# Kernel optimization log

Measured on AMD Instinct MI355X. Metric: run time of the kernel, lower is better.

## Reference

```python
import jax, jax.numpy as jnp
import numpy as np

DIM = 320
HEADS = 8
D_HEAD = 40
CTX_DIM = 768
INNER_FF = 4 * DIM  # 1280
EPS = 1e-5


def _ln(x, w, b):
    mu = jnp.mean(x, axis=-1, keepdims=True)
    var = jnp.mean(jnp.square(x - mu), axis=-1, keepdims=True)
    return (x - mu) * jax.lax.rsqrt(var + EPS) * w + b


def _attn(xq, ctx, Wq, Wk, Wv, Wo, bo):
    # Wq: [dim, inner]; Wk/Wv: [ctx_dim, inner]; Wo: [inner, dim]
    b, n, _ = xq.shape
    m = ctx.shape[1]
    scale = D_HEAD ** -0.5
    q = (xq @ Wq).reshape(b, n, HEADS, D_HEAD)
    k = (ctx @ Wk).reshape(b, m, HEADS, D_HEAD)
    v = (ctx @ Wv).reshape(b, m, HEADS, D_HEAD)
    sim = jnp.einsum('bihd,bjhd->bhij', q, k) * scale
    attn = jax.nn.softmax(sim, axis=-1)
    out = jnp.einsum('bhij,bjhd->bihd', attn, v).reshape(b, n, HEADS * D_HEAD)
    return out @ Wo + bo


def setup_inputs() -> dict:
    key = jax.random.key(0)
    ks = jax.random.split(key, 20)
    s = 0.02
    inner = HEADS * D_HEAD  # 320
    d = {
        'x': jax.random.normal(ks[0], (2, 4096, DIM), jnp.float32),
        'context': jax.random.normal(ks[1], (2, 77, CTX_DIM), jnp.float32),
        # norm params
        'ln1_w': jnp.ones((DIM,)), 'ln1_b': jnp.zeros((DIM,)),
        'ln2_w': jnp.ones((DIM,)), 'ln2_b': jnp.zeros((DIM,)),
        'ln3_w': jnp.ones((DIM,)), 'ln3_b': jnp.zeros((DIM,)),
        # attn1 (self)
        'a1_Wq': jax.random.normal(ks[2], (DIM, inner)) * s,
        'a1_Wk': jax.random.normal(ks[3], (DIM, inner)) * s,
        'a1_Wv': jax.random.normal(ks[4], (DIM, inner)) * s,
        'a1_Wo': jax.random.normal(ks[5], (inner, DIM)) * s,
        'a1_bo': jnp.zeros((DIM,)),
        # attn2 (cross)
        'a2_Wq': jax.random.normal(ks[6], (DIM, inner)) * s,
        'a2_Wk': jax.random.normal(ks[7], (CTX_DIM, inner)) * s,
        'a2_Wv': jax.random.normal(ks[8], (CTX_DIM, inner)) * s,
        'a2_Wo': jax.random.normal(ks[9], (inner, DIM)) * s,
        'a2_bo': jnp.zeros((DIM,)),
        # GEGLU feed-forward
        'ff_W1': jax.random.normal(ks[10], (DIM, 2 * INNER_FF)) * s,
        'ff_b1': jnp.zeros((2 * INNER_FF,)),
        'ff_W2': jax.random.normal(ks[11], (INNER_FF, DIM)) * s,
        'ff_b2': jnp.zeros((DIM,)),
    }
    return d


def reference(x, context, ln1_w, ln1_b, ln2_w, ln2_b, ln3_w, ln3_b,
              a1_Wq, a1_Wk, a1_Wv, a1_Wo, a1_bo,
              a2_Wq, a2_Wk, a2_Wv, a2_Wo, a2_bo,
              ff_W1, ff_b1, ff_W2, ff_b2):
    h = _ln(x, ln1_w, ln1_b)
    x = _attn(h, h, a1_Wq, a1_Wk, a1_Wv, a1_Wo, a1_bo) + x
    h = _ln(x, ln2_w, ln2_b)
    x = _attn(h, context, a2_Wq, a2_Wk, a2_Wv, a2_Wo, a2_bo) + x
    h = _ln(x, ln3_w, ln3_b)
    proj = h @ ff_W1 + ff_b1
    u, gate = jnp.split(proj, 2, axis=-1)
    ff = (u * jax.nn.gelu(gate, approximate=False)) @ ff_W2 + ff_b2
    return ff + x
```

## Files before the change

kernel.cpp:

```cpp
#include <hip/hip_runtime.h>
#include <hip/hip_bf16.h>
#include <math.h>

typedef __hip_bfloat16 bf16;
typedef __attribute__((ext_vector_type(8))) short bf16x8;
typedef __attribute__((ext_vector_type(4))) short bf16x4;
typedef __attribute__((ext_vector_type(4))) float f32x4;
typedef __attribute__((ext_vector_type(2))) unsigned int u32x2;

#define DIM 320
#define HEADS 8
#define DHEAD 40
#define CTXD 768
#define FFI 1280
#define NQ 4096
#define NCTX 77
#define BATCH 2

static __device__ __forceinline__ short f2bs(float v) {
    union { bf16 b; short s; } x; x.b = __float2bfloat16(v); return x.s;
}
static __device__ __forceinline__ unsigned pkbf(float hi, float lo) {
    return __builtin_amdgcn_perm(__float_as_uint(hi), __float_as_uint(lo), 0x07060302u);
}

__global__ void __launch_bounds__(256) wtrans_all(
    const float* q1s, const float* k1s, const float* v1s, const float* o1s,
    const float* q2s, const float* o2s, const float* k2s, const float* v2s,
    const float* w1s, const float* w2s,
    short* q1d, short* k1d, short* v1d, short* o1d,
    short* q2d, short* o2d, short* k2d, short* v2d,
    short* w1d, short* w2d)
{
    int bid = blockIdx.x;
    const float* W; short* Wt; int K, N, base;
    if (bid < 600) {
        int ws = bid / 100; base = bid % 100; K = DIM; N = DIM;
        W  = ws == 0 ? q1s : ws == 1 ? k1s : ws == 2 ? v1s : ws == 3 ? o1s : ws == 4 ? q2s : o2s;
        Wt = ws == 0 ? q1d : ws == 1 ? k1d : ws == 2 ? v1d : ws == 3 ? o1d : ws == 4 ? q2d : o2d;
    } else if (bid < 1080) {
        int i = bid - 600; int ws = i / 240; base = i % 240; K = CTXD; N = DIM;
        W = ws ? v2s : k2s; Wt = ws ? v2d : k2d;
    } else if (bid < 1880) {
        base = bid - 1080; K = DIM; N = 2 * FFI; W = w1s; Wt = w1d;
    } else {
        base = bid - 1880; K = FFI; N = DIM; W = w2s; Wt = w2d;
    }
    int ntx = N / 32;
    int n0 = (base % ntx) * 32, k0 = (base / ntx) * 32;
    __shared__ float T[32][33];
    int c = threadIdx.x & 31, r8 = threadIdx.x >> 5;
#pragma unroll
    for (int rr = 0; rr < 4; ++rr) {
        int r = r8 + rr * 8;
        T[r][c] = W[(size_t)(k0 + r) * N + n0 + c];
    }
    __syncthreads();
#pragma unroll
    for (int rr = 0; rr < 4; ++rr) {
        int r = r8 + rr * 8;
        Wt[(size_t)(n0 + r) * K + k0 + c] = f2bs(T[c][r]);
    }
}

__global__ void __launch_bounds__(256) ln_kernel(const float* __restrict__ src,
                          const float* __restrict__ w, const float* __restrict__ bp,
                          short* __restrict__ out, int rows)
{
    int row = blockIdx.x * 4 + (threadIdx.x >> 6);
    int lane = threadIdx.x & 63;
    if (row >= rows) return;
    float v[5];
    float s = 0.f, s2 = 0.f;
#pragma unroll
    for (int t = 0; t < 5; ++t) {
        int c = lane + t * 64;
        float x = src[(size_t)row * DIM + c];
        v[t] = x; s += x; s2 += x * x;
    }
#pragma unroll
    for (int off = 32; off; off >>= 1) { s += __shfl_xor(s, off); s2 += __shfl_xor(s2, off); }
    float mean = s * (1.f / DIM);
    float var = s2 * (1.f / DIM) - mean * mean;
    float rstd = rsqrtf(var + 1e-5f);
#pragma unroll
    for (int t = 0; t < 5; ++t) {
        int c = lane + t * 64;
        out[(size_t)row * DIM + c] = f2bs((v[t] - mean) * rstd * w[c] + bp[c]);
    }
}

__global__ void __launch_bounds__(256) mfma_qkv(const short* __restrict__ A,
                          const short* __restrict__ wq, const short* __restrict__ wk,
                          const short* __restrict__ wv,
                          short* __restrict__ qb, short* __restrict__ kbuf,
                          short* __restrict__ vts, float qscale)
{
    __shared__ short As[64 * 72];
    __shared__ short Bs[64 * 72];
    const int tid = threadIdx.x;
    const int z = blockIdx.z;
    const short* Wt = z == 0 ? wq : z == 1 ? wk : wv;
    const int w = tid >> 6, lane = tid & 63, lrow = lane & 15, lgrp = lane >> 4;
    const int m0 = blockIdx.y * 64, n0 = blockIdx.x * 64;
    f32x4 acc[4] = {};
    for (int kb = 0; kb < DIM / 64; ++kb) {
        const int k0 = kb << 6;
        __syncthreads();
#pragma unroll
        for (int l = 0; l < 2; ++l) {
            int idx = tid + (l << 8);
            int arow = idx >> 3, ac = idx & 7;
            *(bf16x8*)&As[arow * 72 + ac * 8] =
                *(const bf16x8*)(A + (size_t)(m0 + arow) * DIM + k0 + ac * 8);
            *(bf16x8*)&Bs[arow * 72 + ac * 8] =
                *(const bf16x8*)(Wt + (size_t)(n0 + arow) * DIM + k0 + ac * 8);
        }
        __syncthreads();
#pragma unroll
        for (int s = 0; s < 2; ++s) {
            bf16x8 a = *(const bf16x8*)&As[(w * 16 + lrow) * 72 + s * 32 + lgrp * 8];
#pragma unroll
            for (int ct = 0; ct < 4; ++ct) {
                bf16x8 b = *(const bf16x8*)&Bs[(ct * 16 + lrow) * 72 + s * 32 + lgrp * 8];
                acc[ct] = __builtin_amdgcn_mfma_f32_16x16x32_bf16(a, b, acc[ct], 0, 0, 0);
            }
        }
    }
#pragma unroll
    for (int ct = 0; ct < 4; ++ct) {
        int col = n0 + ct * 16 + lrow;
        if (z == 2) {
            int row0 = m0 + w * 16 + lgrp * 4;
            int b_ = row0 >> 12, kv = row0 & (NQ - 1);
            int hh = col / DHEAD, d = col - hh * DHEAD;
            bf16x4 pv;
#pragma unroll
            for (int r = 0; r < 4; ++r) pv[r] = f2bs(acc[ct][r]);
            *(bf16x4*)(vts + (size_t)((b_ * HEADS + hh) * 48 + d) * NQ + kv) = pv;
        } else {
#pragma unroll
            for (int r = 0; r < 4; ++r) {
                int row = m0 + w * 16 + lgrp * 4 + r;
                float v = acc[ct][r];
                if (z == 0) qb[(size_t)row * DIM + col] = f2bs(v * qscale);
                else        kbuf[(size_t)row * DIM + col] = f2bs(v);
            }
        }
    }
}

__global__ void __launch_bounds__(256) mfma_crosskv(const float* __restrict__ ctx,
                          const short* __restrict__ wk2, const short* __restrict__ wv2,
                          short* __restrict__ k2, short* __restrict__ vt2)
{
    __shared__ short As[64 * 72];
    __shared__ short Bs[64 * 72];
    const int tid = threadIdx.x;
    const int z = blockIdx.z;
    const short* Wt = z ? wv2 : wk2;
    const int Mc = BATCH * NCTX;
    const int w = tid >> 6, lane = tid & 63, lrow = lane & 15, lgrp = lane >> 4;
    const int m0 = blockIdx.y * 64, n0 = blockIdx.x * 64;
    f32x4 acc[4] = {};
    for (int kb = 0; kb < CTXD / 64; ++kb) {
        const int k0 = kb << 6;
        __syncthreads();
#pragma unroll
        for (int l = 0; l < 2; ++l) {
            int idx = tid + (l << 8);
            int arow = idx >> 3, ac = idx & 7;
            int grow = m0 + arow;
            bf16x8 v = {};
            if (grow < Mc) {
                const float* Af = ctx + (size_t)grow * CTXD + k0 + ac * 8;
#pragma unroll
                for (int j = 0; j < 8; ++j) v[j] = f2bs(Af[j]);
            }
            *(bf16x8*)&As[arow * 72 + ac * 8] = v;
            *(bf16x8*)&Bs[arow * 72 + ac * 8] =
                *(const bf16x8*)(Wt + (size_t)(n0 + arow) * CTXD + k0 + ac * 8);
        }
        __syncthreads();
#pragma unroll
        for (int s = 0; s < 2; ++s) {
            bf16x8 a = *(const bf16x8*)&As[(w * 16 + lrow) * 72 + s * 32 + lgrp * 8];
#pragma unroll
            for (int ct = 0; ct < 4; ++ct) {
                bf16x8 b = *(const bf16x8*)&Bs[(ct * 16 + lrow) * 72 + s * 32 + lgrp * 8];
                acc[ct] = __builtin_amdgcn_mfma_f32_16x16x32_bf16(a, b, acc[ct], 0, 0, 0);
            }
        }
    }
#pragma unroll
    for (int ct = 0; ct < 4; ++ct) {
        int col = n0 + ct * 16 + lrow;
#pragma unroll
        for (int r = 0; r < 4; ++r) {
            int row = m0 + w * 16 + lgrp * 4 + r;
            if (row >= Mc) continue;
            float v = acc[ct][r];
            if (z == 0) k2[(size_t)row * DIM + col] = f2bs(v);
            else {
                int b_ = row / NCTX, kv = row - b_ * NCTX;
                int hh = col / DHEAD, d = col - hh * DHEAD;
                vt2[(size_t)((b_ * HEADS + hh) * 48 + d) * 128 + kv] = f2bs(v);
            }
        }
    }
}

template<int MODE>
__global__ void __launch_bounds__(256) mfma_gemm(const short* __restrict__ A,
                          const short* __restrict__ Wt,
                          const float* __restrict__ bias,
                          const float* __restrict__ res,
                          float* __restrict__ xbuf,
                          short* __restrict__ outb,
                          float* __restrict__ outf,
                          int M, int N, int K, float oscale)
{
    __shared__ short As[64 * 72];
    __shared__ short Bs[64 * 72];
    const int tid = threadIdx.x;
    const int w = tid >> 6, lane = tid & 63, lrow = lane & 15, lgrp = lane >> 4;
    const int m0 = blockIdx.y * 64, n0 = blockIdx.x * 64;
    f32x4 acc[4] = {};
    const int kiters = K >> 6;
    for (int kb = 0; kb < kiters; ++kb) {
        const int k0 = kb << 6;
        __syncthreads();
#pragma unroll
        for (int l = 0; l < 2; ++l) {
            int idx = tid + (l << 8);
            int arow = idx >> 3, ac = idx & 7;
            *(bf16x8*)&As[arow * 72 + ac * 8] =
                *(const bf16x8*)(A + (size_t)(m0 + arow) * K + k0 + ac * 8);
            *(bf16x8*)&Bs[arow * 72 + ac * 8] =
                *(const bf16x8*)(Wt + (size_t)(n0 + arow) * K + k0 + ac * 8);
        }
        __syncthreads();
#pragma unroll
        for (int s = 0; s < 2; ++s) {
            bf16x8 a = *(const bf16x8*)&As[(w * 16 + lrow) * 72 + s * 32 + lgrp * 8];
#pragma unroll
            for (int ct = 0; ct < 4; ++ct) {
                bf16x8 b = *(const bf16x8*)&Bs[(ct * 16 + lrow) * 72 + s * 32 + lgrp * 8];
                acc[ct] = __builtin_amdgcn_mfma_f32_16x16x32_bf16(a, b, acc[ct], 0, 0, 0);
            }
        }
    }
#pragma unroll
    for (int ct = 0; ct < 4; ++ct) {
        int col = n0 + ct * 16 + lrow;
        float bvx = bias ? bias[col] : 0.f;
#pragma unroll
        for (int r = 0; r < 4; ++r) {
            int row = m0 + w * 16 + lgrp * 4 + r;
            float v = acc[ct][r] + bvx;
            size_t o = (size_t)row * N + col;
            if (MODE == 0)      outb[o] = f2bs(v * oscale);
            else if (MODE == 1) xbuf[o] = v + res[o];
            else if (MODE == 2) xbuf[o] += v;
            else                outf[o] = v + xbuf[o];
        }
    }
}

__global__ void __launch_bounds__(256) mfma_geglu(const short* __restrict__ A,
                           const short* __restrict__ Wt1,
                           const float* __restrict__ b1, short* __restrict__ G)
{
    __shared__ short As[64 * 72];
    __shared__ short Bu[64 * 72];
    __shared__ short Bg[64 * 72];
    const int tid = threadIdx.x;
    const int w = tid >> 6, lane = tid & 63, lrow = lane & 15, lgrp = lane >> 4;
    const int m0 = blockIdx.y * 64, n0 = blockIdx.x * 64;
    f32x4 au[4] = {}, ag[4] = {};
    for (int kb = 0; kb < DIM / 64; ++kb) {
        const int k0 = kb << 6;
        __syncthreads();
#pragma unroll
        for (int l = 0; l < 2; ++l) {
            int idx = tid + (l << 8);
            int arow = idx >> 3, ac = idx & 7;
            *(bf16x8*)&As[arow * 72 + ac * 8] =
                *(const bf16x8*)(A + (size_t)(m0 + arow) * DIM + k0 + ac * 8);
            *(bf16x8*)&Bu[arow * 72 + ac * 8] =
                *(const bf16x8*)(Wt1 + (size_t)(n0 + arow) * DIM + k0 + ac * 8);
            *(bf16x8*)&Bg[arow * 72 + ac * 8] =
                *(const bf16x8*)(Wt1 + (size_t)(FFI + n0 + arow) * DIM + k0 + ac * 8);
        }
        __syncthreads();
#pragma unroll
        for (int s = 0; s < 2; ++s) {
            bf16x8 a = *(const bf16x8*)&As[(w * 16 + lrow) * 72 + s * 32 + lgrp * 8];
#pragma unroll
            for (int ct = 0; ct < 4; ++ct) {
                bf16x8 bu = *(const bf16x8*)&Bu[(ct * 16 + lrow) * 72 + s * 32 + lgrp * 8];
                au[ct] = __builtin_amdgcn_mfma_f32_16x16x32_bf16(a, bu, au[ct], 0, 0, 0);
                bf16x8 bg = *(const bf16x8*)&Bg[(ct * 16 + lrow) * 72 + s * 32 + lgrp * 8];
                ag[ct] = __builtin_amdgcn_mfma_f32_16x16x32_bf16(a, bg, ag[ct], 0, 0, 0);
            }
        }
    }
#pragma unroll
    for (int ct = 0; ct < 4; ++ct) {
        int col = n0 + ct * 16 + lrow;
        float bu = b1[col], bg = b1[FFI + col];
#pragma unroll
        for (int r = 0; r < 4; ++r) {
            int row = m0 + w * 16 + lgrp * 4 + r;
            float u = au[ct][r] + bu;
            float g = ag[ct][r] + bg;
            float gelu = 0.5f * g * (1.f + erff(g * 0.70710678f));
            G[(size_t)row * FFI + col] = f2bs(u * gelu);
        }
    }
}

template<bool FULL>
__global__ void __launch_bounds__(512) flash_mfma(const short* __restrict__ Q,
                           const short* __restrict__ Kb,
                           const short* __restrict__ VtG,
                           short* __restrict__ O,
                           int kvlen, int kvs)
{
    __shared__ short Ks[2][64 * 64];
    __shared__ short Vt[2][48 * 64];
    __shared__ short Ps[128 * 64];
    const int tid = threadIdx.x;
    const int w = tid >> 6, lane = tid & 63, lrow = lane & 15, lgrp = lane >> 4;
    const int hh = blockIdx.y, b = blockIdx.z;
    const int q0 = blockIdx.x * 128;
    const int swz = (lrow & 7) << 4;

    if (tid < 512) { ((bf16x8*)Ks[0])[tid] = (bf16x8){}; ((bf16x8*)Ks[1])[tid] = (bf16x8){}; }
    if (tid < 384) {
        short fill = ((tid >> 3) == 40) ? (short)0x3F80 : (short)0;
        bf16x8 f8 = {fill, fill, fill, fill, fill, fill, fill, fill};
        ((bf16x8*)Vt[0])[tid] = f8; ((bf16x8*)Vt[1])[tid] = f8;
    }

    const size_t qbase = ((size_t)(b * NQ + q0 + w * 16 + lrow)) * DIM + hh * DHEAD;
    bf16x8 bq0 = *(const bf16x8*)(Q + qbase + lgrp * 8);
    bf16x8 bq1 = {};
    if (lgrp == 0) bq1 = *(const bf16x8*)(Q + qbase + 32);

    const bool isK = tid < 320;
    const int kv0 = isK ? tid / 5 : 0, cc0 = isK ? tid % 5 : 0;
    const int vc0 = tid - 320;
    const int vd0 = vc0 >> 3, vcc0 = vc0 & 7;
    const bool hasV1 = tid < 192;
    const int vd1 = (192 + tid) >> 3, vcc1 = (192 + tid) & 7;
    const bool wrV1 = hasV1 && (vd1 < DHEAD);

    bf16x8 st0, st1;
    const size_t kbase = (size_t)b * kvlen;
    const size_t vbase = (size_t)((b * HEADS + hh) * 48);

    auto issue = [&](int t) {
        const int j0 = t << 6;
        st0 = (bf16x8){};
        if (isK) {
            if (FULL || j0 + kv0 < kvlen)
                st0 = *(const bf16x8*)(Kb + (kbase + j0 + kv0) * DIM + hh * DHEAD + cc0 * 8);
        } else {
            st0 = *(const bf16x8*)(VtG + (vbase + vd0) * kvs + j0 + vcc0 * 8);
            if (!FULL && j0 + 63 >= kvlen) {
#pragma unroll
                for (int j = 0; j < 8; ++j) if (j0 + vcc0 * 8 + j >= kvlen) st0[j] = 0;
            }
        }
        if (wrV1) {
            st1 = *(const bf16x8*)(VtG + (vbase + vd1) * kvs + j0 + vcc1 * 8);
            if (!FULL && j0 + 63 >= kvlen) {
#pragma unroll
                for (int j = 0; j < 8; ++j) if (j0 + vcc1 * 8 + j >= kvlen) st1[j] = 0;
            }
        }
    };
    auto commit = [&](int bi) {
        if (isK)
            *(bf16x8*)((char*)Ks[bi] + kv0 * 128 + ((cc0 * 16) ^ ((kv0 & 7) << 4))) = st0;
        else
            *(bf16x8*)((char*)Vt[bi] + vd0 * 128 + ((vcc0 * 16) ^ ((vd0 & 7) << 4))) = st0;
        if (wrV1)
            *(bf16x8*)((char*)Vt[bi] + vd1 * 128 + ((vcc1 * 16) ^ ((vd1 & 7) << 4))) = st1;
    };

    f32x4 o_acc[3] = {};

    issue(0);
    __syncthreads();
    commit(0);
    const int ntiles = (kvlen + 63) >> 6;
    char* prow = (char*)Ps + (w * 16 + lrow) * 128;
    for (int t = 0; t < ntiles; ++t) {
        const int j0 = t << 6;
        const int bi = t & 1;
        __syncthreads();
        if (t + 1 < ntiles) issue(t + 1);

        f32x4 sacc[4] = {};
#pragma unroll
        for (int ct = 0; ct < 4; ++ct) {
            const char* krow = (char*)Ks[bi] + (ct * 16 + lrow) * 128;
            bf16x8 ak0 = *(const bf16x8*)(krow + ((lgrp * 16) ^ swz));
            sacc[ct] = __builtin_amdgcn_mfma_f32_16x16x32_bf16(ak0, bq0, sacc[ct], 0, 0, 0);
            bf16x8 ak1 = *(const bf16x8*)(krow + ((64 + lgrp * 16) ^ swz));
            sacc[ct] = __builtin_amdgcn_mfma_f32_16x16x32_bf16(ak1, bq1, sacc[ct], 0, 0, 0);
        }
        if (!FULL && j0 + 64 > kvlen) {
#pragma unroll
            for (int ct = 0; ct < 4; ++ct)
#pragma unroll
                for (int r = 0; r < 4; ++r)
                    if (j0 + ct * 16 + lgrp * 4 + r >= kvlen) sacc[ct][r] = -1e30f;
        }
#pragma unroll
        for (int ct = 0; ct < 4; ++ct) {
            float p0 = __builtin_amdgcn_exp2f(sacc[ct][0]);
            float p1 = __builtin_amdgcn_exp2f(sacc[ct][1]);
            float p2 = __builtin_amdgcn_exp2f(sacc[ct][2]);
            float p3 = __builtin_amdgcn_exp2f(sacc[ct][3]);
            u32x2 pk; pk[0] = pkbf(p1, p0); pk[1] = pkbf(p3, p2);
            *(u32x2*)(prow + ((ct * 32 + lgrp * 8) ^ swz)) = pk;
        }
#pragma unroll
        for (int s = 0; s < 2; ++s) {
            bf16x8 bp = *(const bf16x8*)(prow + ((s * 64 + lgrp * 16) ^ swz));
#pragma unroll
            for (int dt = 0; dt < 3; ++dt) {
                bf16x8 av = *(const bf16x8*)((char*)Vt[bi] + (dt * 16 + lrow) * 128 + ((s * 64 + lgrp * 16) ^ swz));
                o_acc[dt] = __builtin_amdgcn_mfma_f32_16x16x32_bf16(av, bp, o_acc[dt], 0, 0, 0);
            }
        }
        if (t + 1 < ntiles) commit((t + 1) & 1);
    }
    float lsum = __shfl(o_acc[2][0], 32 + (lane & 15));
    float invl = 1.f / lsum;
    const size_t obase = ((size_t)(b * NQ + q0 + w * 16 + lrow)) * DIM + hh * DHEAD;
#pragma unroll
    for (int dt = 0; dt < 3; ++dt) {
        int dbase = dt * 16 + lgrp * 4;
        if (dbase < DHEAD) {
            u32x2 ov;
            ov[0] = pkbf(o_acc[dt][1] * invl, o_acc[dt][0] * invl);
            ov[1] = pkbf(o_acc[dt][3] * invl, o_acc[dt][2] * invl);
            *(u32x2*)(O + obase + dbase) = ov;
        }
    }
}

extern "C" void kernel_launch(void* const* d_in, const int* in_sizes, int n_in,
                              void* d_out, int out_size, void* d_ws, size_t ws_size,
                              hipStream_t stream)
{
    const float* x      = (const float*)d_in[0];
    const float* ctx    = (const float*)d_in[1];
    const float* ln1_w  = (const float*)d_in[2];
    const float* ln1_b  = (const float*)d_in[3];
    const float* ln2_w  = (const float*)d_in[4];
    const float* ln2_b  = (const float*)d_in[5];
    const float* ln3_w  = (const float*)d_in[6];
    const float* ln3_b  = (const float*)d_in[7];
    const float* a1_Wq  = (const float*)d_in[8];
    const float* a1_Wk  = (const float*)d_in[9];
    const float* a1_Wv  = (const float*)d_in[10];
    const float* a1_Wo  = (const float*)d_in[11];
    const float* a1_bo  = (const float*)d_in[12];
    const float* a2_Wq  = (const float*)d_in[13];
    const float* a2_Wk  = (const float*)d_in[14];
    const float* a2_Wv  = (const float*)d_in[15];
    const float* a2_Wo  = (const float*)d_in[16];
    const float* a2_bo  = (const float*)d_in[17];
    const float* ff_W1  = (const float*)d_in[18];
    const float* ff_b1  = (const float*)d_in[19];
    const float* ff_W2  = (const float*)d_in[20];
    const float* ff_b2  = (const float*)d_in[21];

    const int M = BATCH * NQ;
    const float qscale2 = (float)(0.15811388300841898 * 1.4426950408889634);

    char* p = (char*)d_ws;
    auto carve = [&](size_t bytes) { char* r = p; p += (bytes + 255) & ~255ULL; return r; };
    short* h       = (short*)carve((size_t)M * DIM * 2);
    short* qb      = (short*)carve((size_t)M * DIM * 2);
    short* kbuf    = (short*)carve((size_t)M * DIM * 2);
    short* attnout = (short*)carve((size_t)M * DIM * 2);
    float* xbuf    = (float*)carve((size_t)M * DIM * 4);
    short* gbuf    = (short*)carve((size_t)M * FFI * 2);
    short* VtS     = (short*)carve((size_t)BATCH * HEADS * 48 * NQ * 2);
    short* Vt2     = (short*)carve((size_t)BATCH * HEADS * 48 * 128 * 2);
    short* k2      = (short*)carve((size_t)256 * DIM * 2);
    short* wtq1    = (short*)carve((size_t)DIM * DIM * 2);
    short* wtk1    = (short*)carve((size_t)DIM * DIM * 2);
    short* wtv1    = (short*)carve((size_t)DIM * DIM * 2);
    short* wto1    = (short*)carve((size_t)DIM * DIM * 2);
    short* wtq2    = (short*)carve((size_t)DIM * DIM * 2);
    short* wto2    = (short*)carve((size_t)DIM * DIM * 2);
    short* wtk2    = (short*)carve((size_t)DIM * CTXD * 2);
    short* wtv2    = (short*)carve((size_t)DIM * CTXD * 2);
    short* wt1     = (short*)carve((size_t)2 * FFI * DIM * 2);
    short* wt2     = (short*)carve((size_t)DIM * FFI * 2);

    dim3 blk(256);
    dim3 g320(DIM / 64, M / 64);
    dim3 gattn(NQ / 128, HEADS, BATCH);

    wtrans_all<<<2280, blk, 0, stream>>>(a1_Wq, a1_Wk, a1_Wv, a1_Wo, a2_Wq, a2_Wo,
                                         a2_Wk, a2_Wv, ff_W1, ff_W2,
                                         wtq1, wtk1, wtv1, wto1, wtq2, wto2,
                                         wtk2, wtv2, wt1, wt2);
    ln_kernel<<<M / 4, blk, 0, stream>>>(x, ln1_w, ln1_b, h, M);
    mfma_qkv<<<dim3(5, 128, 3), blk, 0, stream>>>(h, wtq1, wtk1, wtv1, qb, kbuf, VtS, qscale2);
    flash_mfma<true><<<gattn, dim3(512), 0, stream>>>(qb, kbuf, VtS, attnout, NQ, NQ);
    mfma_gemm<1><<<g320, blk, 0, stream>>>(attnout, wto1, a1_bo, x, xbuf, nullptr, nullptr, M, DIM, DIM, 1.f);
    ln_kernel<<<M / 4, blk, 0, stream>>>(xbuf, ln2_w, ln2_b, h, M);
    mfma_gemm<0><<<g320, blk, 0, stream>>>(h, wtq2, nullptr, nullptr, nullptr, qb, nullptr, M, DIM, DIM, qscale2);
    mfma_crosskv<<<dim3(5, 3, 2), blk, 0, stream>>>(ctx, wtk2, wtv2, k2, Vt2);
    flash_mfma<false><<<gattn, dim3(512), 0, stream>>>(qb, k2, Vt2, attnout, NCTX, 128);
    mfma_gemm<2><<<g320, blk, 0, stream>>>(attnout, wto2, a2_bo, nullptr, xbuf, nullptr, nullptr, M, DIM, DIM, 1.f);
    ln_kernel<<<M / 4, blk, 0, stream>>>(xbuf, ln3_w, ln3_b, h, M);
    mfma_geglu<<<dim3(FFI / 64, M / 64), blk, 0, stream>>>(h, wt1, ff_b1, gbuf);
    mfma_gemm<3><<<g320, blk, 0, stream>>>(gbuf, wt2, ff_b2, nullptr, xbuf, nullptr, (float*)d_out, M, DIM, FFI, 1.f);
}
```

Before: 249.3 us.

## Enlarge GEMM tiles to 128x64 with 2x2 wave layout; add MFMA priority hints

All dense GEMM kernels (QKV, output projections, GEGLU, FF2) move from 64x64 tiles, where each wave computed a 16x64 strip, to 128x64 tiles. Waves are now arranged 2x2 and each computes a 64x32 sub-tile, so B fragments are reused across four A fragments and the M grid is halved. This is meant to cut global and LDS traffic per MFMA, at the cost of more accumulator registers and fewer blocks. The flash attention kernel also raises wave priority around its MFMA sections using s_setprio.

```diff
diff --git a/kernel.cpp b/kernel.cpp
--- a/kernel.cpp
+++ b/kernel.cpp
@@ -90,61 +90,203 @@
     }
 }
 
-__global__ void __launch_bounds__(256) mfma_qkv(const short* __restrict__ A,
+
+template<int MODE>
+__global__ void __launch_bounds__(256) gemm128(const short* __restrict__ A,
+                          const short* __restrict__ Wt,
+                          const float* __restrict__ bias,
+                          const float* __restrict__ res,
+                          float* __restrict__ xbuf,
+                          short* __restrict__ outb,
+                          float* __restrict__ outf,
+                          int N, int K, float oscale)
+{
+    __shared__ short As[128 * 72];
+    __shared__ short Bs[64 * 72];
+    const int tid = threadIdx.x;
+    const int w = tid >> 6, lane = tid & 63, lrow = lane & 15, lgrp = lane >> 4;
+    const int wr = w >> 1, wc = w & 1;
+    const int m0 = blockIdx.y * 128, n0 = blockIdx.x * 64;
+    f32x4 acc[4][2] = {};
+    for (int k0 = 0; k0 < K; k0 += 64) {
+        __syncthreads();
+#pragma unroll
+        for (int l = 0; l < 4; ++l) {
+            int idx = tid + (l << 8);
+            int arow = idx >> 3, ac = idx & 7;
+            *(bf16x8*)&As[arow * 72 + ac * 8] =
+                *(const bf16x8*)(A + (size_t)(m0 + arow) * K + k0 + ac * 8);
+        }
+#pragma unroll
+        for (int l = 0; l < 2; ++l) {
+            int idx = tid + (l << 8);
+            int brow = idx >> 3, bc = idx & 7;
+            *(bf16x8*)&Bs[brow * 72 + bc * 8] =
+                *(const bf16x8*)(Wt + (size_t)(n0 + brow) * K + k0 + bc * 8);
+        }
+        __syncthreads();
+#pragma unroll
+        for (int s = 0; s < 2; ++s) {
+            bf16x8 b0 = *(const bf16x8*)&Bs[(wc * 32 + lrow) * 72 + s * 32 + lgrp * 8];
+            bf16x8 b1 = *(const bf16x8*)&Bs[(wc * 32 + 16 + lrow) * 72 + s * 32 + lgrp * 8];
+#pragma unroll
+            for (int m = 0; m < 4; ++m) {
+                bf16x8 a = *(const bf16x8*)&As[(wr * 64 + m * 16 + lrow) * 72 + s * 32 + lgrp * 8];
+                acc[m][0] = __builtin_amdgcn_mfma_f32_16x16x32_bf16(a, b0, acc[m][0], 0, 0, 0);
+                acc[m][1] = __builtin_amdgcn_mfma_f32_16x16x32_bf16(a, b1, acc[m][1], 0, 0, 0);
+            }
+        }
+    }
+#pragma unroll
+    for (int n = 0; n < 2; ++n) {
+        int col = n0 + wc * 32 + n * 16 + lrow;
+        float bvx = bias ? bias[col] : 0.f;
+#pragma unroll
+        for (int m = 0; m < 4; ++m) {
+#pragma unroll
+            for (int r = 0; r < 4; ++r) {
+                int row = m0 + wr * 64 + m * 16 + lgrp * 4 + r;
+                float v = acc[m][n][r] + bvx;
+                size_t o = (size_t)row * N + col;
+                if (MODE == 0)      outb[o] = f2bs(v * oscale);
+                else if (MODE == 1) xbuf[o] = v + res[o];
+                else if (MODE == 2) xbuf[o] += v;
+                else                outf[o] = v + xbuf[o];
+            }
+        }
+    }
+}
+
+__global__ void __launch_bounds__(256) qkv128(const short* __restrict__ A,
                           const short* __restrict__ wq, const short* __restrict__ wk,
                           const short* __restrict__ wv,
                           short* __restrict__ qb, short* __restrict__ kbuf,
                           short* __restrict__ vts, float qscale)
 {
-    __shared__ short As[64 * 72];
+    __shared__ short As[128 * 72];
     __shared__ short Bs[64 * 72];
     const int tid = threadIdx.x;
     const int z = blockIdx.z;
     const short* Wt = z == 0 ? wq : z == 1 ? wk : wv;
     const int w = tid >> 6, lane = tid & 63, lrow = lane & 15, lgrp = lane >> 4;
-    const int m0 = blockIdx.y * 64, n0 = blockIdx.x * 64;
-    f32x4 acc[4] = {};
-    for (int kb = 0; kb < DIM / 64; ++kb) {
-        const int k0 = kb << 6;
-        __syncthreads();
-#pragma unroll
-        for (int l = 0; l < 2; ++l) {
+    const int wr = w >> 1, wc = w & 1;
+    const int m0 = blockIdx.y * 128, n0 = blockIdx.x * 64;
+    f32x4 acc[4][2] = {};
+    for (int k0 = 0; k0 < DIM; k0 += 64) {
+        __syncthreads();
+#pragma unroll
+        for (int l = 0; l < 4; ++l) {
             int idx = tid + (l << 8);
             int arow = idx >> 3, ac = idx & 7;
             *(bf16x8*)&As[arow * 72 + ac * 8] =
                 *(const bf16x8*)(A + (size_t)(m0 + arow) * DIM + k0 + ac * 8);
-            *(bf16x8*)&Bs[arow * 72 + ac * 8] =
-                *(const bf16x8*)(Wt + (size_t)(n0 + arow) * DIM + k0 + ac * 8);
+        }
+#pragma unroll
+        for (int l = 0; l < 2; ++l) {
+            int idx = tid + (l << 8);
+            int brow = idx >> 3, bc = idx & 7;
+            *(bf16x8*)&Bs[brow * 72 + bc * 8] =
+                *(const bf16x8*)(Wt + (size_t)(n0 + brow) * DIM + k0 + bc * 8);
         }
         __syncthreads();
 #pragma unroll
         for (int s = 0; s < 2; ++s) {
-            bf16x8 a = *(const bf16x8*)&As[(w * 16 + lrow) * 72 + s * 32 + lgrp * 8];
-#pragma unroll
-            for (int ct = 0; ct < 4; ++ct) {
-                bf16x8 b = *(const bf16x8*)&Bs[(ct * 16 + lrow) * 72 + s * 32 + lgrp * 8];
-                acc[ct] = __builtin_amdgcn_mfma_f32_16x16x32_bf16(a, b, acc[ct], 0, 0, 0);
-            }
-        }
-    }
-#pragma unroll
-    for (int ct = 0; ct < 4; ++ct) {
-        int col = n0 + ct * 16 + lrow;
-        if (z == 2) {
-            int row0 = m0 + w * 16 + lgrp * 4;
-            int b_ = row0 >> 12, kv = row0 & (NQ - 1);
-            int hh = col / DHEAD, d = col - hh * DHEAD;
-            bf16x4 pv;
-#pragma unroll
-            for (int r = 0; r < 4; ++r) pv[r] = f2bs(acc[ct][r]);
-            *(bf16x4*)(vts + (size_t)((b_ * HEADS + hh) * 48 + d) * NQ + kv) = pv;
-        } else {
+            bf16x8 b0 = *(const bf16x8*)&Bs[(wc * 32 + lrow) * 72 + s * 32 + lgrp * 8];
+            bf16x8 b1 = *(const bf16x8*)&Bs[(wc * 32 + 16 + lrow) * 72 + s * 32 + lgrp * 8];
+#pragma unroll
+            for (int m = 0; m < 4; ++m) {
+                bf16x8 a = *(const bf16x8*)&As[(wr * 64 + m * 16 + lrow) * 72 + s * 32 + lgrp * 8];
+                acc[m][0] = __builtin_amdgcn_mfma_f32_16x16x32_bf16(a, b0, acc[m][0], 0, 0, 0);
+                acc[m][1] = __builtin_amdgcn_mfma_f32_16x16x32_bf16(a, b1, acc[m][1], 0, 0, 0);
+            }
+        }
+    }
+#pragma unroll
+    for (int n = 0; n < 2; ++n) {
+        int col = n0 + wc * 32 + n * 16 + lrow;
+#pragma unroll
+        for (int m = 0; m < 4; ++m) {
+            if (z == 2) {
+                int row0 = m0 + wr * 64 + m * 16 + lgrp * 4;
+                int b_ = row0 >> 12, kv = row0 & (NQ - 1);
+                int hh = col / DHEAD, d = col - hh * DHEAD;
+                bf16x4 pv;
+#pragma unroll
+                for (int r = 0; r < 4; ++r) pv[r] = f2bs(acc[m][n][r]);
+                *(bf16x4*)(vts + (size_t)((b_ * HEADS + hh) * 48 + d) * NQ + kv) = pv;
+            } else {
+#pragma unroll
+                for (int r = 0; r < 4; ++r) {
+                    int row = m0 + wr * 64 + m * 16 + lgrp * 4 + r;
+                    float v = acc[m][n][r];
+                    if (z == 0) qb[(size_t)row * DIM + col] = f2bs(v * qscale);
+                    else        kbuf[(size_t)row * DIM + col] = f2bs(v);
+                }
+            }
+        }
+    }
+}
+
+__global__ void __launch_bounds__(256) geglu128(const short* __restrict__ A,
+                           const short* __restrict__ Wt1,
+                           const float* __restrict__ b1, short* __restrict__ G)
+{
+    __shared__ short As[128 * 72];
+    __shared__ short Bu[64 * 72];
+    __shared__ short Bg[64 * 72];
+    const int tid = threadIdx.x;
+    const int w = tid >> 6, lane = tid & 63, lrow = lane & 15, lgrp = lane >> 4;
+    const int wr = w >> 1, wc = w & 1;
+    const int m0 = blockIdx.y * 128, n0 = blockIdx.x * 64;
+    f32x4 au[4][2] = {}, ag[4][2] = {};
+    for (int k0 = 0; k0 < DIM; k0 += 64) {
+        __syncthreads();
+#pragma unroll
+        for (int l = 0; l < 4; ++l) {
+            int idx = tid + (l << 8);
+            int arow = idx >> 3, ac = idx & 7;
+            *(bf16x8*)&As[arow * 72 + ac * 8] =
+                *(const bf16x8*)(A + (size_t)(m0 + arow) * DIM + k0 + ac * 8);
+        }
+#pragma unroll
+        for (int l = 0; l < 2; ++l) {
+            int idx = tid + (l << 8);
+            int brow = idx >> 3, bc = idx & 7;
+            *(bf16x8*)&Bu[brow * 72 + bc * 8] =
+                *(const bf16x8*)(Wt1 + (size_t)(n0 + brow) * DIM + k0 + bc * 8);
+            *(bf16x8*)&Bg[brow * 72 + bc * 8] =
+                *(const bf16x8*)(Wt1 + (size_t)(FFI + n0 + brow) * DIM + k0 + bc * 8);
+        }
+        __syncthreads();
+#pragma unroll
+        for (int s = 0; s < 2; ++s) {
+            bf16x8 bu0 = *(const bf16x8*)&Bu[(wc * 32 + lrow) * 72 + s * 32 + lgrp * 8];
+            bf16x8 bu1 = *(const bf16x8*)&Bu[(wc * 32 + 16 + lrow) * 72 + s * 32 + lgrp * 8];
+            bf16x8 bg0 = *(const bf16x8*)&Bg[(wc * 32 + lrow) * 72 + s * 32 + lgrp * 8];
+            bf16x8 bg1 = *(const bf16x8*)&Bg[(wc * 32 + 16 + lrow) * 72 + s * 32 + lgrp * 8];
+#pragma unroll
+            for (int m = 0; m < 4; ++m) {
+                bf16x8 a = *(const bf16x8*)&As[(wr * 64 + m * 16 + lrow) * 72 + s * 32 + lgrp * 8];
+                au[m][0] = __builtin_amdgcn_mfma_f32_16x16x32_bf16(a, bu0, au[m][0], 0, 0, 0);
+                au[m][1] = __builtin_amdgcn_mfma_f32_16x16x32_bf16(a, bu1, au[m][1], 0, 0, 0);
+                ag[m][0] = __builtin_amdgcn_mfma_f32_16x16x32_bf16(a, bg0, ag[m][0], 0, 0, 0);
+                ag[m][1] = __builtin_amdgcn_mfma_f32_16x16x32_bf16(a, bg1, ag[m][1], 0, 0, 0);
+            }
+        }
+    }
+#pragma unroll
+    for (int n = 0; n < 2; ++n) {
+        int col = n0 + wc * 32 + n * 16 + lrow;
+        float bu = b1[col], bg = b1[FFI + col];
+#pragma unroll
+        for (int m = 0; m < 4; ++m) {
 #pragma unroll
             for (int r = 0; r < 4; ++r) {
-                int row = m0 + w * 16 + lgrp * 4 + r;
-                float v = acc[ct][r];
-                if (z == 0) qb[(size_t)row * DIM + col] = f2bs(v * qscale);
-                else        kbuf[(size_t)row * DIM + col] = f2bs(v);
+                int row = m0 + wr * 64 + m * 16 + lgrp * 4 + r;
+                float u = au[m][n][r] + bu;
+                float g = ag[m][n][r] + bg;
+                float gelu = 0.5f * g * (1.f + erff(g * 0.70710678f));
+                G[(size_t)row * FFI + col] = f2bs(u * gelu);
             }
         }
     }
@@ -210,116 +352,6 @@
     }
 }
 
-template<int MODE>
-__global__ void __launch_bounds__(256) mfma_gemm(const short* __restrict__ A,
-                          const short* __restrict__ Wt,
-                          const float* __restrict__ bias,
-                          const float* __restrict__ res,
-                          float* __restrict__ xbuf,
-                          short* __restrict__ outb,
-                          float* __restrict__ outf,
-                          int M, int N, int K, float oscale)
-{
-    __shared__ short As[64 * 72];
-    __shared__ short Bs[64 * 72];
-    const int tid = threadIdx.x;
-    const int w = tid >> 6, lane = tid & 63, lrow = lane & 15, lgrp = lane >> 4;
-    const int m0 = blockIdx.y * 64, n0 = blockIdx.x * 64;
-    f32x4 acc[4] = {};
-    const int kiters = K >> 6;
-    for (int kb = 0; kb < kiters; ++kb) {
-        const int k0 = kb << 6;
-        __syncthreads();
-#pragma unroll
-        for (int l = 0; l < 2; ++l) {
-            int idx = tid + (l << 8);
-            int arow = idx >> 3, ac = idx & 7;
-            *(bf16x8*)&As[arow * 72 + ac * 8] =
-                *(const bf16x8*)(A + (size_t)(m0 + arow) * K + k0 + ac * 8);
-            *(bf16x8*)&Bs[arow * 72 + ac * 8] =
-                *(const bf16x8*)(Wt + (size_t)(n0 + arow) * K + k0 + ac * 8);
-        }
-        __syncthreads();
-#pragma unroll
-        for (int s = 0; s < 2; ++s) {
-            bf16x8 a = *(const bf16x8*)&As[(w * 16 + lrow) * 72 + s * 32 + lgrp * 8];
-#pragma unroll
-            for (int ct = 0; ct < 4; ++ct) {
-                bf16x8 b = *(const bf16x8*)&Bs[(ct * 16 + lrow) * 72 + s * 32 + lgrp * 8];
-                acc[ct] = __builtin_amdgcn_mfma_f32_16x16x32_bf16(a, b, acc[ct], 0, 0, 0);
-            }
-        }
-    }
-#pragma unroll
-    for (int ct = 0; ct < 4; ++ct) {
-        int col = n0 + ct * 16 + lrow;
-        float bvx = bias ? bias[col] : 0.f;
-#pragma unroll
-        for (int r = 0; r < 4; ++r) {
-            int row = m0 + w * 16 + lgrp * 4 + r;
-            float v = acc[ct][r] + bvx;
-            size_t o = (size_t)row * N + col;
-            if (MODE == 0)      outb[o] = f2bs(v * oscale);
-            else if (MODE == 1) xbuf[o] = v + res[o];
-            else if (MODE == 2) xbuf[o] += v;
-            else                outf[o] = v + xbuf[o];
-        }
-    }
-}
-
-__global__ void __launch_bounds__(256) mfma_geglu(const short* __restrict__ A,
-                           const short* __restrict__ Wt1,
-                           const float* __restrict__ b1, short* __restrict__ G)
-{
-    __shared__ short As[64 * 72];
-    __shared__ short Bu[64 * 72];
-    __shared__ short Bg[64 * 72];
-    const int tid = threadIdx.x;
-    const int w = tid >> 6, lane = tid & 63, lrow = lane & 15, lgrp = lane >> 4;
-    const int m0 = blockIdx.y * 64, n0 = blockIdx.x * 64;
-    f32x4 au[4] = {}, ag[4] = {};
-    for (int kb = 0; kb < DIM / 64; ++kb) {
-        const int k0 = kb << 6;
-        __syncthreads();
-#pragma unroll
-        for (int l = 0; l < 2; ++l) {
-            int idx = tid + (l << 8);
-            int arow = idx >> 3, ac = idx & 7;
-            *(bf16x8*)&As[arow * 72 + ac * 8] =
-                *(const bf16x8*)(A + (size_t)(m0 + arow) * DIM + k0 + ac * 8);
-            *(bf16x8*)&Bu[arow * 72 + ac * 8] =
-                *(const bf16x8*)(Wt1 + (size_t)(n0 + arow) * DIM + k0 + ac * 8);
-            *(bf16x8*)&Bg[arow * 72 + ac * 8] =
-                *(const bf16x8*)(Wt1 + (size_t)(FFI + n0 + arow) * DIM + k0 + ac * 8);
-        }
-        __syncthreads();
-#pragma unroll
-        for (int s = 0; s < 2; ++s) {
-            bf16x8 a = *(const bf16x8*)&As[(w * 16 + lrow) * 72 + s * 32 + lgrp * 8];
-#pragma unroll
-            for (int ct = 0; ct < 4; ++ct) {
-                bf16x8 bu = *(const bf16x8*)&Bu[(ct * 16 + lrow) * 72 + s * 32 + lgrp * 8];
-                au[ct] = __builtin_amdgcn_mfma_f32_16x16x32_bf16(a, bu, au[ct], 0, 0, 0);
-                bf16x8 bg = *(const bf16x8*)&Bg[(ct * 16 + lrow) * 72 + s * 32 + lgrp * 8];
-                ag[ct] = __builtin_amdgcn_mfma_f32_16x16x32_bf16(a, bg, ag[ct], 0, 0, 0);
-            }
-        }
-    }
-#pragma unroll
-    for (int ct = 0; ct < 4; ++ct) {
-        int col = n0 + ct * 16 + lrow;
-        float bu = b1[col], bg = b1[FFI + col];
-#pragma unroll
-        for (int r = 0; r < 4; ++r) {
-            int row = m0 + w * 16 + lgrp * 4 + r;
-            float u = au[ct][r] + bu;
-            float g = ag[ct][r] + bg;
-            float gelu = 0.5f * g * (1.f + erff(g * 0.70710678f));
-            G[(size_t)row * FFI + col] = f2bs(u * gelu);
-        }
-    }
-}
-
 template<bool FULL>
 __global__ void __launch_bounds__(512) flash_mfma(const short* __restrict__ Q,
                            const short* __restrict__ Kb,
@@ -404,6 +436,7 @@
         if (t + 1 < ntiles) issue(t + 1);
 
         f32x4 sacc[4] = {};
+        __builtin_amdgcn_s_setprio(1);
 #pragma unroll
         for (int ct = 0; ct < 4; ++ct) {
             const char* krow = (char*)Ks[bi] + (ct * 16 + lrow) * 128;
@@ -412,6 +445,7 @@
             bf16x8 ak1 = *(const bf16x8*)(krow + ((64 + lgrp * 16) ^ swz));
             sacc[ct] = __builtin_amdgcn_mfma_f32_16x16x32_bf16(ak1, bq1, sacc[ct], 0, 0, 0);
         }
+        __builtin_amdgcn_s_setprio(0);
         if (!FULL && j0 + 64 > kvlen) {
 #pragma unroll
             for (int ct = 0; ct < 4; ++ct)
@@ -428,6 +462,7 @@
             u32x2 pk; pk[0] = pkbf(p1, p0); pk[1] = pkbf(p3, p2);
             *(u32x2*)(prow + ((ct * 32 + lgrp * 8) ^ swz)) = pk;
         }
+        __builtin_amdgcn_s_setprio(1);
 #pragma unroll
         for (int s = 0; s < 2; ++s) {
             bf16x8 bp = *(const bf16x8*)(prow + ((s * 64 + lgrp * 16) ^ swz));
@@ -437,6 +472,7 @@
                 o_acc[dt] = __builtin_amdgcn_mfma_f32_16x16x32_bf16(av, bp, o_acc[dt], 0, 0, 0);
             }
         }
+        __builtin_amdgcn_s_setprio(0);
         if (t + 1 < ntiles) commit((t + 1) & 1);
     }
     float lsum = __shfl(o_acc[2][0], 32 + (lane & 15));
@@ -507,7 +543,7 @@
     short* wt2     = (short*)carve((size_t)DIM * FFI * 2);
 
     dim3 blk(256);
-    dim3 g320(DIM / 64, M / 64);
+    dim3 g128(DIM / 64, M / 128);
     dim3 gattn(NQ / 128, HEADS, BATCH);
 
     wtrans_all<<<2280, blk, 0, stream>>>(a1_Wq, a1_Wk, a1_Wv, a1_Wo, a2_Wq, a2_Wo,
@@ -515,15 +551,15 @@
                                          wtq1, wtk1, wtv1, wto1, wtq2, wto2,
                                          wtk2, wtv2, wt1, wt2);
     ln_kernel<<<M / 4, blk, 0, stream>>>(x, ln1_w, ln1_b, h, M);
-    mfma_qkv<<<dim3(5, 128, 3), blk, 0, stream>>>(h, wtq1, wtk1, wtv1, qb, kbuf, VtS, qscale2);
+    qkv128<<<dim3(5, 64, 3), blk, 0, stream>>>(h, wtq1, wtk1, wtv1, qb, kbuf, VtS, qscale2);
     flash_mfma<true><<<gattn, dim3(512), 0, stream>>>(qb, kbuf, VtS, attnout, NQ, NQ);
-    mfma_gemm<1><<<g320, blk, 0, stream>>>(attnout, wto1, a1_bo, x, xbuf, nullptr, nullptr, M, DIM, DIM, 1.f);
+    gemm128<1><<<g128, blk, 0, stream>>>(attnout, wto1, a1_bo, x, xbuf, nullptr, nullptr, DIM, DIM, 1.f);
     ln_kernel<<<M / 4, blk, 0, stream>>>(xbuf, ln2_w, ln2_b, h, M);
-    mfma_gemm<0><<<g320, blk, 0, stream>>>(h, wtq2, nullptr, nullptr, nullptr, qb, nullptr, M, DIM, DIM, qscale2);
+    gemm128<0><<<g128, blk, 0, stream>>>(h, wtq2, nullptr, nullptr, nullptr, qb, nullptr, DIM, DIM, qscale2);
     mfma_crosskv<<<dim3(5, 3, 2), blk, 0, stream>>>(ctx, wtk2, wtv2, k2, Vt2);
     flash_mfma<false><<<gattn, dim3(512), 0, stream>>>(qb, k2, Vt2, attnout, NCTX, 128);
-    mfma_gemm<2><<<g320, blk, 0, stream>>>(attnout, wto2, a2_bo, nullptr, xbuf, nullptr, nullptr, M, DIM, DIM, 1.f);
+    gemm128<2><<<g128, blk, 0, stream>>>(attnout, wto2, a2_bo, nullptr, xbuf, nullptr, nullptr, DIM, DIM, 1.f);
     ln_kernel<<<M / 4, blk, 0, stream>>>(xbuf, ln3_w, ln3_b, h, M);
-    mfma_geglu<<<dim3(FFI / 64, M / 64), blk, 0, stream>>>(h, wt1, ff_b1, gbuf);
-    mfma_gemm<3><<<g320, blk, 0, stream>>>(gbuf, wt2, ff_b2, nullptr, xbuf, nullptr, (float*)d_out, M, DIM, FFI, 1.f);
-}
+    geglu128<<<dim3(FFI / 64, M / 128), blk, 0, stream>>>(h, wt1, ff_b1, gbuf);
+    gemm128<3><<<g128, blk, 0, stream>>>(gbuf, wt2, ff_b2, nullptr, xbuf, nullptr, (float*)d_out, DIM, FFI, 1.f);
+}
```

After: 239.5 us. 1.04x faster.
